# Kernel tuning notes

Measured on AMD Instinct MI355X. Metric: run time of the kernel, lower is better.

The kernel has to match this reference:

```python
import jax, jax.numpy as jnp
import numpy as np

N = 100000      # n_nodes
D = 64          # in_features == out_features (elementwise W mul requires equality)
DEG = 16        # avg degree for random edges
H = 2           # n_head
ALPHA = 0.2     # LeakyReLU negative slope


def setup_inputs() -> dict:
    key = jax.random.key(0)
    k1, k2, k3 = jax.random.split(key, 3)
    inputs = jax.random.normal(k1, (N, D), dtype=jnp.float32)
    # random edges + self-loops so every row has at least one edge (nonzero rowsum)
    rnd = jax.random.randint(k2, (2, N * DEG), 0, N)
    self_loops = jnp.tile(jnp.arange(N)[None, :], (2, 1))
    edge_index = jnp.concatenate([self_loops, rnd], axis=1)  # [2, 1.7M]
    # per-head params, matching torch init: W = ones, a ~ U(-stdv, stdv)
    W = jnp.ones((H, D), dtype=jnp.float32)
    stdv = 1.0 / np.sqrt(D * 2)
    a = jax.random.uniform(k3, (H, 2 * D), dtype=jnp.float32, minval=-stdv, maxval=stdv)
    return {"inputs": inputs, "edge_index": edge_index, "W": W, "a": a}


def reference(inputs, edge_index, W, a):
    n = inputs.shape[0]
    row, col = edge_index[0], edge_index[1]

    def head(Wh, ah):
        h = inputs * Wh  # [N, D]
        # a @ [h_src; h_dst] decomposes into per-node dots, then scalar edge gather
        score = (h @ ah[:D])[row] + (h @ ah[D:])[col]          # [E]
        e = jnp.exp(jnp.where(score > 0, score, ALPHA * score))  # exp(leaky_relu)
        rowsum = jax.ops.segment_sum(e, row, num_segments=n)     # [N]
        # sparse.mm(coo(edge, e), inputs): h_prime[i] = sum_j e_ij * inputs[j]
        h_prime = jax.ops.segment_sum(e[:, None] * inputs[col], row, num_segments=n)
        return h_prime / rowsum[:, None]

    outs = jax.vmap(head)(W, a)  # [H, N, D]
    return outs.mean(axis=0)
```

## Files before the change

kernel.cpp:

```cpp
#include <hip/hip_runtime.h>
#include <hip/hip_fp16.h>


#define D 64
#define ALPHA 0.2f
#define BSHIFT 8
#define BROWS 256
#define MAXBUK 512
#define TILE 2048
#define PK2 17
#define M17 ((1u << PK2) - 1u)
#define CAPE 6144

__device__ __forceinline__ unsigned bf16rne(float f) {
    unsigned u = __float_as_uint(f);
    u += 0x7fffu + ((u >> 16) & 1u);
    return u >> 16;
}
__device__ __forceinline__ float lrexp(float sc) {
    return __expf(sc > 0.f ? sc : ALPHA * sc);
}
__device__ __forceinline__ unsigned packe(float e0, float e1) {
    __half2 h = __floats2half2_rn(e0, e1);
    return *reinterpret_cast<unsigned*>(&h);
}
__device__ __forceinline__ float2 unpacke(unsigned u) {
    __half2 h = *reinterpret_cast<__half2*>(&u);
    return __half22float2(h);
}

__global__ __launch_bounds__(256) void k_front(
    const float* __restrict__ x, const float* __restrict__ W,
    const float* __restrict__ a, float4* __restrict__ s,
    unsigned* __restrict__ xh2, const int* __restrict__ row,
    unsigned short* __restrict__ tcnt, int N, int E, int nblkA)
{
    __shared__ int h[MAXBUK];
    if ((int)blockIdx.x < nblkA) {
        int wid  = (blockIdx.x * 256 + threadIdx.x) >> 6;
        int lane = threadIdx.x & 63;
        int node = wid * 4 + (lane >> 4);
        int f4   = lane & 15;
        if (node >= N) return;
        const float4* x4 = (const float4*)x;
        const float4* W4 = (const float4*)W;
        const float4* A4 = (const float4*)a;
        float4 v  = x4[(size_t)node * 16 + f4];
        unsigned u01 = (bf16rne(v.y) << 16) | bf16rne(v.x);
        unsigned u23 = (bf16rne(v.w) << 16) | bf16rne(v.z);
        *(uint2*)(xh2 + (size_t)node * 32 + 2 * f4) = make_uint2(u01, u23);
        float4 w0 = W4[f4], w1 = W4[16 + f4];
        float4 a0 = A4[f4], a1 = A4[16 + f4], a2 = A4[32 + f4], a3 = A4[48 + f4];
        float4 h0 = make_float4(v.x * w0.x, v.y * w0.y, v.z * w0.z, v.w * w0.w);
        float4 h1 = make_float4(v.x * w1.x, v.y * w1.y, v.z * w1.z, v.w * w1.w);
        float t0 = h0.x * a0.x + h0.y * a0.y + h0.z * a0.z + h0.w * a0.w;
        float t1 = h0.x * a1.x + h0.y * a1.y + h0.z * a1.z + h0.w * a1.w;
        float t2 = h1.x * a2.x + h1.y * a2.y + h1.z * a2.z + h1.w * a2.w;
        float t3 = h1.x * a3.x + h1.y * a3.y + h1.z * a3.z + h1.w * a3.w;
#pragma unroll
        for (int off = 1; off < 16; off <<= 1) {
            t0 += __shfl_xor(t0, off);
            t1 += __shfl_xor(t1, off);
            t2 += __shfl_xor(t2, off);
            t3 += __shfl_xor(t3, off);
        }
        if (f4 == 0) s[node] = make_float4(t0, t1, t2, t3);
    } else {
        int tile = blockIdx.x - nblkA;
        int t = threadIdx.x, base = tile * TILE;
        int cnt = E - base; if (cnt > TILE) cnt = TILE;
        h[t] = 0; h[t + 256] = 0;
        __syncthreads();
        for (int i = t; i < cnt; i += 256) atomicAdd(&h[row[base + i] >> BSHIFT], 1);
        __syncthreads();
        tcnt[(size_t)tile * MAXBUK + t]       = (unsigned short)h[t];
        tcnt[(size_t)tile * MAXBUK + t + 256] = (unsigned short)h[t + 256];
    }
}

__global__ __launch_bounds__(256) void k_col_scan(
    const unsigned short* __restrict__ tcnt, int* __restrict__ tbase,
    int* __restrict__ bcnt, int NT, int nbuk)
{
    int b = blockIdx.x, t = threadIdx.x;
    if (b >= nbuk) { if (t == 0) bcnt[b] = 0; return; }
    __shared__ int wsum[256];
    int t4 = t * 4;
    int v0 = (t4     < NT) ? tcnt[(size_t)(t4    ) * MAXBUK + b] : 0;
    int v1 = (t4 + 1 < NT) ? tcnt[(size_t)(t4 + 1) * MAXBUK + b] : 0;
    int v2 = (t4 + 2 < NT) ? tcnt[(size_t)(t4 + 2) * MAXBUK + b] : 0;
    int v3 = (t4 + 3 < NT) ? tcnt[(size_t)(t4 + 3) * MAXBUK + b] : 0;
    int sv = v0 + v1 + v2 + v3;
    wsum[t] = sv;
    __syncthreads();
    for (int off = 1; off < 256; off <<= 1) {
        int add = (t >= off) ? wsum[t - off] : 0;
        __syncthreads();
        wsum[t] += add;
        __syncthreads();
    }
    int run = wsum[t] - sv;
    if (t4     < NT) { tbase[(size_t)(t4    ) * MAXBUK + b] = run; run += v0; }
    if (t4 + 1 < NT) { tbase[(size_t)(t4 + 1) * MAXBUK + b] = run; run += v1; }
    if (t4 + 2 < NT) { tbase[(size_t)(t4 + 2) * MAXBUK + b] = run; run += v2; }
    if (t4 + 3 < NT) { tbase[(size_t)(t4 + 3) * MAXBUK + b] = run; run += v3; }
    if (t == 255) bcnt[b] = wsum[255];
}

__global__ __launch_bounds__(256) void k_binning(
    const int* __restrict__ row, const int* __restrict__ col,
    const unsigned short* __restrict__ tcnt, const int* __restrict__ bcnt,
    const int* __restrict__ tbase, unsigned* __restrict__ ebuf,
    int* __restrict__ bbase_g, int E)
{
    __shared__ int lrow[TILE];
    __shared__ int lcol[TILE];
    __shared__ int st[MAXBUK];
    __shared__ int gb[MAXBUK];
    __shared__ int cur[MAXBUK];
    __shared__ int w2[256];
    int t = threadIdx.x;
    int tile = blockIdx.x;
    int base = tile * TILE;
    int cnt = E - base; if (cnt > TILE) cnt = TILE;

    int h0 = tcnt[(size_t)tile * MAXBUK + 2 * t];
    int h1 = tcnt[(size_t)tile * MAXBUK + 2 * t + 1];
    int sv = h0 + h1;
    w2[t] = sv;
    __syncthreads();
    for (int off = 1; off < 256; off <<= 1) {
        int add = (t >= off) ? w2[t - off] : 0;
        __syncthreads();
        w2[t] += add;
        __syncthreads();
    }
    int run = w2[t] - sv;
    st[2 * t] = run;       st[2 * t + 1] = run + h0;
    cur[2 * t] = run;      cur[2 * t + 1] = run + h0;
    __syncthreads();

    int b0 = bcnt[2 * t], b1 = bcnt[2 * t + 1];
    int sb = b0 + b1;
    w2[t] = sb;
    __syncthreads();
    for (int off = 1; off < 256; off <<= 1) {
        int add = (t >= off) ? w2[t - off] : 0;
        __syncthreads();
        w2[t] += add;
        __syncthreads();
    }
    int runb = w2[t] - sb;
    gb[2 * t]     = runb      + tbase[(size_t)tile * MAXBUK + 2 * t];
    gb[2 * t + 1] = runb + b0 + tbase[(size_t)tile * MAXBUK + 2 * t + 1];
    if (tile == 0) {
        bbase_g[2 * t] = runb; bbase_g[2 * t + 1] = runb + b0;
        if (t == 255) bbase_g[512] = runb + b0 + b1;
    }
    __syncthreads();

    for (int i = t; i < cnt; i += 256) {
        int r = row[base + i], c = col[base + i];
        int p = atomicAdd(&cur[r >> BSHIFT], 1);
        lrow[p] = r; lcol[p] = c;
    }
    __syncthreads();

    for (int i = t; i < cnt; i += 256) {
        int rr = lrow[i];
        int bb = rr >> BSHIFT;
        ebuf[gb[bb] + (i - st[bb])] =
            ((unsigned)(rr & (BROWS - 1)) << PK2) | (unsigned)lcol[i];
    }
}

__global__ __launch_bounds__(1024) void k_rowsort(
    const unsigned* __restrict__ ebuf, const int* __restrict__ bbase,
    const float4* __restrict__ s, int* __restrict__ offsets,
    int* __restrict__ counts, unsigned* __restrict__ scol,
    __half* __restrict__ ecoef, int N)
{
    __shared__ unsigned lpk[CAPE];
    __shared__ unsigned lev[CAPE];
    __shared__ int   hist[BROWS];
    __shared__ int   offs[BROWS];
    __shared__ int   cursor[BROWS];
    __shared__ float rs0[BROWS], rs1[BROWS];
    __shared__ float rsx[BROWS], rsz[BROWS];
    __shared__ int   wsum[256];
    int b = blockIdx.x, t = threadIdx.x;
    int lo = b << BSHIFT;
    int s0 = bbase[b], s1 = bbase[b + 1];
    int seg = s1 - s0;

    if (t < BROWS) {
        int g = lo + t;
        float4 f = (g < N) ? s[g] : make_float4(0.f, 0.f, 0.f, 0.f);
        rsx[t] = f.x; rsz[t] = f.z;
        hist[t] = 0; rs0[t] = 0.f; rs1[t] = 0.f;
    }
    __syncthreads();

    for (int i = s0 + t; i < s1; i += 1024)
        atomicAdd(&hist[ebuf[i] >> PK2], 1);
    __syncthreads();

    int a = 0;
    if (t < BROWS) { a = hist[t]; wsum[t] = a; }
    __syncthreads();
    for (int off = 1; off < 256; off <<= 1) {
        int add = 0;
        if (t < BROWS && t >= off) add = wsum[t - off];
        __syncthreads();
        if (t < BROWS) wsum[t] += add;
        __syncthreads();
    }
    if (t < BROWS) { offs[t] = wsum[t] - a; cursor[t] = wsum[t] - a; }
    __syncthreads();

    if (seg <= CAPE) {
        for (int i = s0 + t; i < s1; i += 1024) {
            unsigned pk = ebuf[i];
            int r = pk >> PK2, c = (int)(pk & M17);
            float4 sc = s[c];
            float e0 = lrexp(rsx[r] + sc.y);
            float e1 = lrexp(rsz[r] + sc.w);
            atomicAdd(&rs0[r], e0);
            atomicAdd(&rs1[r], e1);
            int p = atomicAdd(&cursor[r], 1);
            lpk[p] = pk; lev[p] = packe(e0, e1);
        }
        __syncthreads();
        if (t < BROWS) {
            rs0[t] = 0.5f / rs0[t]; rs1[t] = 0.5f / rs1[t];
            int rg = lo + t;
            if (rg < N) { offsets[rg] = s0 + offs[t]; counts[rg] = hist[t]; }
        }
        __syncthreads();
        for (int i = t; i < seg; i += 1024) {
            unsigned pk = lpk[i];
            int r = pk >> PK2;
            float2 ef = unpacke(lev[i]);
            float coef = rs0[r] * ef.x + rs1[r] * ef.y;
            scol[s0 + i]  = (pk & M17) << 5;
            ecoef[s0 + i] = __float2half(coef);
        }
    } else {
        for (int i = s0 + t; i < s1; i += 1024) {
            unsigned pk = ebuf[i];
            int r = pk >> PK2, c = (int)(pk & M17);
            float4 sc = s[c];
            atomicAdd(&rs0[r], lrexp(rsx[r] + sc.y));
            atomicAdd(&rs1[r], lrexp(rsz[r] + sc.w));
        }
        __syncthreads();
        if (t < BROWS) {
            rs0[t] = 0.5f / rs0[t]; rs1[t] = 0.5f / rs1[t];
            int rg = lo + t;
            if (rg < N) { offsets[rg] = s0 + offs[t]; counts[rg] = hist[t]; }
        }
        __syncthreads();
        for (int i = s0 + t; i < s1; i += 1024) {
            unsigned pk = ebuf[i];
            int r = pk >> PK2, c = (int)(pk & M17);
            float4 sc = s[c];
            float coef = rs0[r] * lrexp(rsx[r] + sc.y)
                       + rs1[r] * lrexp(rsz[r] + sc.w);
            int p = atomicAdd(&cursor[r], 1);
            scol[s0 + p]  = (unsigned)c << 5;
            ecoef[s0 + p] = __float2half(coef);
        }
    }
}

__global__ __launch_bounds__(256) void k_gather(
    const unsigned* __restrict__ xh2, const int* __restrict__ offsets,
    const int* __restrict__ counts, const unsigned* __restrict__ scol,
    const __half* __restrict__ ecoef, float* __restrict__ out, int N)
{
    int w    = threadIdx.x >> 6;
    int lane = threadIdx.x & 63;
    int n    = blockIdx.x * 4 + w;
    if (n >= N) return;
    int start = offsets[n], cnt = counts[n];
    int q  = lane >> 4;
    int li = lane & 15;
    float a0 = 0.f, a1 = 0.f, a2 = 0.f, a3 = 0.f;
    for (int kk = q; kk < cnt; kk += 4) {
        unsigned cb = scol[start + kk];
        float cf = __half2float(ecoef[start + kk]);
        uint2 u = *(const uint2*)(xh2 + cb + 2 * li);
        a0 += cf * __uint_as_float(u.x << 16);
        a1 += cf * __uint_as_float(u.x & 0xffff0000u);
        a2 += cf * __uint_as_float(u.y << 16);
        a3 += cf * __uint_as_float(u.y & 0xffff0000u);
    }
    a0 += __shfl_xor(a0, 16); a0 += __shfl_xor(a0, 32);
    a1 += __shfl_xor(a1, 16); a1 += __shfl_xor(a1, 32);
    a2 += __shfl_xor(a2, 16); a2 += __shfl_xor(a2, 32);
    a3 += __shfl_xor(a3, 16); a3 += __shfl_xor(a3, 32);
    if (q == 0)
        ((float4*)(out + (size_t)n * D))[li] = make_float4(a0, a1, a2, a3);
}

extern "C" void kernel_launch(void* const* d_in, const int* in_sizes, int n_in,
                              void* d_out, int out_size, void* d_ws, size_t ws_size,
                              hipStream_t stream)
{
    const float* x  = (const float*)d_in[0];
    const int*   ei = (const int*)d_in[1];
    const float* W  = (const float*)d_in[2];
    const float* a  = (const float*)d_in[3];
    float*       out = (float*)d_out;
    int N = in_sizes[0] / D;
    int E = in_sizes[1] / 2;
    const int* row = ei;
    const int* col = ei + E;

    int NBUK = (N + BROWS - 1) >> BSHIFT;
    int NT   = (E + TILE - 1) / TILE;

    uintptr_t wp = (uintptr_t)d_ws;
    auto alloc = [&wp](size_t bytes) -> void* {
        wp = (wp + 255) & ~(uintptr_t)255;
        void* p = (void*)wp;
        wp += bytes;
        return p;
    };
    unsigned*       xh2     = (unsigned*)alloc((size_t)N * 32 * 4);
    float4*         s       = (float4*)alloc((size_t)N * sizeof(float4));
    int*            offsets = (int*)alloc((size_t)N * sizeof(int));
    int*            counts  = (int*)alloc((size_t)N * sizeof(int));
    unsigned*       scol    = (unsigned*)alloc((size_t)E * sizeof(unsigned));
    unsigned*       ebuf    = (unsigned*)alloc((size_t)E * sizeof(unsigned));
    __half*         ecoef   = (__half*)alloc((size_t)E * sizeof(__half));
    int*            tbase   = (int*)alloc((size_t)NT * MAXBUK * sizeof(int));
    int*            bcnt    = (int*)alloc(MAXBUK * sizeof(int));
    int*            bbase   = (int*)alloc((MAXBUK + 4) * sizeof(int));
    unsigned short* tcnt    = (unsigned short*)alloc((size_t)NT * MAXBUK * 2);

    int nblkA = (N + 15) / 16;
    k_front<<<nblkA + NT, 256, 0, stream>>>(x, W, a, s, xh2, row, tcnt, N, E, nblkA);
    k_col_scan<<<MAXBUK, 256, 0, stream>>>(tcnt, tbase, bcnt, NT, NBUK);
    k_binning<<<NT, 256, 0, stream>>>(row, col, tcnt, bcnt, tbase, ebuf, bbase, E);
    k_rowsort<<<NBUK, 1024, 0, stream>>>(ebuf, bbase, s, offsets, counts, scol, ecoef, N);
    k_gather<<<(N + 3) / 4, 256, 0, stream>>>(xh2, offsets, counts, scol, ecoef, out, N);
}
```

Before: 199.2 us.

## Drop global column scan; gather bucket segments per tile and stage neighbors in LDS

```diff
diff --git a/kernel.cpp b/kernel.cpp
--- a/kernel.cpp
+++ b/kernel.cpp
@@ -4,6 +4,7 @@
 
 #define D 64
 #define ALPHA 0.2f
+#define CAP 96
 #define BSHIFT 8
 #define BROWS 256
 #define MAXBUK 512
@@ -11,6 +12,7 @@
 #define PK2 17
 #define M17 ((1u << PK2) - 1u)
 #define CAPE 6144
+#define SSTR 8192
 
 __device__ __forceinline__ unsigned bf16rne(float f) {
     unsigned u = __float_as_uint(f);
@@ -51,12 +53,10 @@
         *(uint2*)(xh2 + (size_t)node * 32 + 2 * f4) = make_uint2(u01, u23);
         float4 w0 = W4[f4], w1 = W4[16 + f4];
         float4 a0 = A4[f4], a1 = A4[16 + f4], a2 = A4[32 + f4], a3 = A4[48 + f4];
-        float4 h0 = make_float4(v.x * w0.x, v.y * w0.y, v.z * w0.z, v.w * w0.w);
-        float4 h1 = make_float4(v.x * w1.x, v.y * w1.y, v.z * w1.z, v.w * w1.w);
-        float t0 = h0.x * a0.x + h0.y * a0.y + h0.z * a0.z + h0.w * a0.w;
-        float t1 = h0.x * a1.x + h0.y * a1.y + h0.z * a1.z + h0.w * a1.w;
-        float t2 = h1.x * a2.x + h1.y * a2.y + h1.z * a2.z + h1.w * a2.w;
-        float t3 = h1.x * a3.x + h1.y * a3.y + h1.z * a3.z + h1.w * a3.w;
+        float t0 = v.x*w0.x*a0.x + v.y*w0.y*a0.y + v.z*w0.z*a0.z + v.w*w0.w*a0.w;
+        float t1 = v.x*w0.x*a1.x + v.y*w0.y*a1.y + v.z*w0.z*a1.z + v.w*w0.w*a1.w;
+        float t2 = v.x*w1.x*a2.x + v.y*w1.y*a2.y + v.z*w1.z*a2.z + v.w*w1.w*a2.w;
+        float t3 = v.x*w1.x*a3.x + v.y*w1.y*a3.y + v.z*w1.z*a3.z + v.w*w1.w*a3.w;
 #pragma unroll
         for (int off = 1; off < 16; off <<= 1) {
             t0 += __shfl_xor(t0, off);
@@ -78,120 +78,58 @@
     }
 }
 
-__global__ __launch_bounds__(256) void k_col_scan(
-    const unsigned short* __restrict__ tcnt, int* __restrict__ tbase,
-    int* __restrict__ bcnt, int NT, int nbuk)
-{
-    int b = blockIdx.x, t = threadIdx.x;
-    if (b >= nbuk) { if (t == 0) bcnt[b] = 0; return; }
-    __shared__ int wsum[256];
-    int t4 = t * 4;
-    int v0 = (t4     < NT) ? tcnt[(size_t)(t4    ) * MAXBUK + b] : 0;
-    int v1 = (t4 + 1 < NT) ? tcnt[(size_t)(t4 + 1) * MAXBUK + b] : 0;
-    int v2 = (t4 + 2 < NT) ? tcnt[(size_t)(t4 + 2) * MAXBUK + b] : 0;
-    int v3 = (t4 + 3 < NT) ? tcnt[(size_t)(t4 + 3) * MAXBUK + b] : 0;
-    int sv = v0 + v1 + v2 + v3;
-    wsum[t] = sv;
-    __syncthreads();
-    for (int off = 1; off < 256; off <<= 1) {
-        int add = (t >= off) ? wsum[t - off] : 0;
-        __syncthreads();
-        wsum[t] += add;
-        __syncthreads();
-    }
-    int run = wsum[t] - sv;
-    if (t4     < NT) { tbase[(size_t)(t4    ) * MAXBUK + b] = run; run += v0; }
-    if (t4 + 1 < NT) { tbase[(size_t)(t4 + 1) * MAXBUK + b] = run; run += v1; }
-    if (t4 + 2 < NT) { tbase[(size_t)(t4 + 2) * MAXBUK + b] = run; run += v2; }
-    if (t4 + 3 < NT) { tbase[(size_t)(t4 + 3) * MAXBUK + b] = run; run += v3; }
-    if (t == 255) bcnt[b] = wsum[255];
-}
-
 __global__ __launch_bounds__(256) void k_binning(
     const int* __restrict__ row, const int* __restrict__ col,
-    const unsigned short* __restrict__ tcnt, const int* __restrict__ bcnt,
-    const int* __restrict__ tbase, unsigned* __restrict__ ebuf,
-    int* __restrict__ bbase_g, int E)
-{
-    __shared__ int lrow[TILE];
-    __shared__ int lcol[TILE];
-    __shared__ int st[MAXBUK];
-    __shared__ int gb[MAXBUK];
+    const unsigned short* __restrict__ tcnt, unsigned* __restrict__ ebuf,
+    unsigned* __restrict__ tmeta, int E)
+{
+    __shared__ unsigned lpk[TILE];
     __shared__ int cur[MAXBUK];
-    __shared__ int w2[256];
-    int t = threadIdx.x;
-    int tile = blockIdx.x;
-    int base = tile * TILE;
+    __shared__ int wsum[256];
+    int t = threadIdx.x, tile = blockIdx.x, base = tile * TILE;
     int cnt = E - base; if (cnt > TILE) cnt = TILE;
 
     int h0 = tcnt[(size_t)tile * MAXBUK + 2 * t];
     int h1 = tcnt[(size_t)tile * MAXBUK + 2 * t + 1];
     int sv = h0 + h1;
-    w2[t] = sv;
+    wsum[t] = sv;
     __syncthreads();
     for (int off = 1; off < 256; off <<= 1) {
-        int add = (t >= off) ? w2[t - off] : 0;
-        __syncthreads();
-        w2[t] += add;
-        __syncthreads();
-    }
-    int run = w2[t] - sv;
-    st[2 * t] = run;       st[2 * t + 1] = run + h0;
-    cur[2 * t] = run;      cur[2 * t + 1] = run + h0;
-    __syncthreads();
-
-    int b0 = bcnt[2 * t], b1 = bcnt[2 * t + 1];
-    int sb = b0 + b1;
-    w2[t] = sb;
-    __syncthreads();
-    for (int off = 1; off < 256; off <<= 1) {
-        int add = (t >= off) ? w2[t - off] : 0;
-        __syncthreads();
-        w2[t] += add;
-        __syncthreads();
-    }
-    int runb = w2[t] - sb;
-    gb[2 * t]     = runb      + tbase[(size_t)tile * MAXBUK + 2 * t];
-    gb[2 * t + 1] = runb + b0 + tbase[(size_t)tile * MAXBUK + 2 * t + 1];
-    if (tile == 0) {
-        bbase_g[2 * t] = runb; bbase_g[2 * t + 1] = runb + b0;
-        if (t == 255) bbase_g[512] = runb + b0 + b1;
-    }
+        int add = (t >= off) ? wsum[t - off] : 0;
+        __syncthreads();
+        wsum[t] += add;
+        __syncthreads();
+    }
+    int run = wsum[t] - sv;
+    cur[2 * t] = run;  cur[2 * t + 1] = run + h0;
+    tmeta[(size_t)tile * MAXBUK + 2 * t]     = ((unsigned)run << 16) | (unsigned)h0;
+    tmeta[(size_t)tile * MAXBUK + 2 * t + 1] = ((unsigned)(run + h0) << 16) | (unsigned)h1;
     __syncthreads();
 
     for (int i = t; i < cnt; i += 256) {
         int r = row[base + i], c = col[base + i];
         int p = atomicAdd(&cur[r >> BSHIFT], 1);
-        lrow[p] = r; lcol[p] = c;
-    }
-    __syncthreads();
-
-    for (int i = t; i < cnt; i += 256) {
-        int rr = lrow[i];
-        int bb = rr >> BSHIFT;
-        ebuf[gb[bb] + (i - st[bb])] =
-            ((unsigned)(rr & (BROWS - 1)) << PK2) | (unsigned)lcol[i];
-    }
+        lpk[p] = ((unsigned)(r & (BROWS - 1)) << PK2) | (unsigned)c;
+    }
+    __syncthreads();
+    for (int i = t; i < cnt; i += 256) ebuf[base + i] = lpk[i];
 }
 
 __global__ __launch_bounds__(1024) void k_rowsort(
-    const unsigned* __restrict__ ebuf, const int* __restrict__ bbase,
+    const unsigned* __restrict__ ebuf, const unsigned* __restrict__ tmeta,
     const float4* __restrict__ s, int* __restrict__ offsets,
     int* __restrict__ counts, unsigned* __restrict__ scol,
-    __half* __restrict__ ecoef, int N)
-{
-    __shared__ unsigned lpk[CAPE];
-    __shared__ unsigned lev[CAPE];
-    __shared__ int   hist[BROWS];
-    __shared__ int   offs[BROWS];
-    __shared__ int   cursor[BROWS];
-    __shared__ float rs0[BROWS], rs1[BROWS];
-    __shared__ float rsx[BROWS], rsz[BROWS];
+    __half* __restrict__ ecoef, int NT, int N)
+{
+    __shared__ unsigned lpkA[CAPE];
+    __shared__ unsigned lpkB[CAPE];
+    __shared__ unsigned levB[CAPE];
+    __shared__ int   hist[BROWS], offs[BROWS], cursor[BROWS];
+    __shared__ float rs0[BROWS], rs1[BROWS], rsx[BROWS], rsz[BROWS];
     __shared__ int   wsum[256];
+    __shared__ int   top;
     int b = blockIdx.x, t = threadIdx.x;
     int lo = b << BSHIFT;
-    int s0 = bbase[b], s1 = bbase[b + 1];
-    int seg = s1 - s0;
 
     if (t < BROWS) {
         int g = lo + t;
@@ -199,28 +137,41 @@
         rsx[t] = f.x; rsz[t] = f.z;
         hist[t] = 0; rs0[t] = 0.f; rs1[t] = 0.f;
     }
-    __syncthreads();
-
-    for (int i = s0 + t; i < s1; i += 1024)
-        atomicAdd(&hist[ebuf[i] >> PK2], 1);
-    __syncthreads();
-
-    int a = 0;
-    if (t < BROWS) { a = hist[t]; wsum[t] = a; }
-    __syncthreads();
-    for (int off = 1; off < 256; off <<= 1) {
-        int add = 0;
-        if (t < BROWS && t >= off) add = wsum[t - off];
-        __syncthreads();
-        if (t < BROWS) wsum[t] += add;
-        __syncthreads();
-    }
-    if (t < BROWS) { offs[t] = wsum[t] - a; cursor[t] = wsum[t] - a; }
-    __syncthreads();
+    if (t == 0) top = 0;
+    __syncthreads();
+
+    int myh = 0, mybase = 0, mydst = 0;
+    if (t < NT) {
+        unsigned m = tmeta[(size_t)t * MAXBUK + b];
+        myh = (int)(m & 0xffffu);
+        mybase = t * TILE + (int)(m >> 16);
+        if (myh) mydst = atomicAdd(&top, myh);
+    }
+    __syncthreads();
+    int seg = top;
+    size_t ob = (size_t)b * SSTR;
 
     if (seg <= CAPE) {
-        for (int i = s0 + t; i < s1; i += 1024) {
-            unsigned pk = ebuf[i];
+        for (int j = 0; j < myh; j++) {
+            unsigned pk = ebuf[mybase + j];
+            lpkA[mydst + j] = pk;
+            atomicAdd(&hist[pk >> PK2], 1);
+        }
+        __syncthreads();
+        int a = 0;
+        if (t < 256) { a = hist[t]; wsum[t] = a; }
+        __syncthreads();
+        for (int off = 1; off < 256; off <<= 1) {
+            int add = 0;
+            if (t < 256 && t >= off) add = wsum[t - off];
+            __syncthreads();
+            if (t < 256) wsum[t] += add;
+            __syncthreads();
+        }
+        if (t < 256) { offs[t] = wsum[t] - a; cursor[t] = wsum[t] - a; }
+        __syncthreads();
+        for (int i = t; i < seg; i += 1024) {
+            unsigned pk = lpkA[i];
             int r = pk >> PK2, c = (int)(pk & M17);
             float4 sc = s[c];
             float e0 = lrexp(rsx[r] + sc.y);
@@ -228,47 +179,61 @@
             atomicAdd(&rs0[r], e0);
             atomicAdd(&rs1[r], e1);
             int p = atomicAdd(&cursor[r], 1);
-            lpk[p] = pk; lev[p] = packe(e0, e1);
+            lpkB[p] = pk; levB[p] = packe(e0, e1);
         }
         __syncthreads();
         if (t < BROWS) {
             rs0[t] = 0.5f / rs0[t]; rs1[t] = 0.5f / rs1[t];
             int rg = lo + t;
-            if (rg < N) { offsets[rg] = s0 + offs[t]; counts[rg] = hist[t]; }
+            if (rg < N) { offsets[rg] = (int)ob + offs[t]; counts[rg] = hist[t]; }
         }
         __syncthreads();
         for (int i = t; i < seg; i += 1024) {
-            unsigned pk = lpk[i];
+            unsigned pk = lpkB[i];
             int r = pk >> PK2;
-            float2 ef = unpacke(lev[i]);
-            float coef = rs0[r] * ef.x + rs1[r] * ef.y;
-            scol[s0 + i]  = (pk & M17) << 5;
-            ecoef[s0 + i] = __float2half(coef);
+            float2 ef = unpacke(levB[i]);
+            scol[ob + i]  = (pk & M17) << 5;
+            ecoef[ob + i] = __float2half(rs0[r] * ef.x + rs1[r] * ef.y);
         }
     } else {
-        for (int i = s0 + t; i < s1; i += 1024) {
-            unsigned pk = ebuf[i];
+        for (int j = 0; j < myh; j++) {
+            unsigned pk = ebuf[mybase + j];
             int r = pk >> PK2, c = (int)(pk & M17);
             float4 sc = s[c];
             atomicAdd(&rs0[r], lrexp(rsx[r] + sc.y));
             atomicAdd(&rs1[r], lrexp(rsz[r] + sc.w));
-        }
+            atomicAdd(&hist[r], 1);
+        }
+        __syncthreads();
+        int a = 0;
+        if (t < 256) { a = hist[t]; wsum[t] = a; }
+        __syncthreads();
+        for (int off = 1; off < 256; off <<= 1) {
+            int add = 0;
+            if (t < 256 && t >= off) add = wsum[t - off];
+            __syncthreads();
+            if (t < 256) wsum[t] += add;
+            __syncthreads();
+        }
+        if (t < 256) { offs[t] = wsum[t] - a; cursor[t] = wsum[t] - a; }
         __syncthreads();
         if (t < BROWS) {
             rs0[t] = 0.5f / rs0[t]; rs1[t] = 0.5f / rs1[t];
             int rg = lo + t;
-            if (rg < N) { offsets[rg] = s0 + offs[t]; counts[rg] = hist[t]; }
-        }
-        __syncthreads();
-        for (int i = s0 + t; i < s1; i += 1024) {
-            unsigned pk = ebuf[i];
+            if (rg < N) { offsets[rg] = (int)ob + offs[t]; counts[rg] = hist[t]; }
+        }
+        __syncthreads();
+        for (int j = 0; j < myh; j++) {
+            unsigned pk = ebuf[mybase + j];
             int r = pk >> PK2, c = (int)(pk & M17);
             float4 sc = s[c];
             float coef = rs0[r] * lrexp(rsx[r] + sc.y)
                        + rs1[r] * lrexp(rsz[r] + sc.w);
             int p = atomicAdd(&cursor[r], 1);
-            scol[s0 + p]  = (unsigned)c << 5;
-            ecoef[s0 + p] = __float2half(coef);
+            if ((unsigned)p < SSTR) {
+                scol[ob + p]  = (unsigned)(pk & M17) << 5;
+                ecoef[ob + p] = __float2half(coef);
+            }
         }
     }
 }
@@ -278,17 +243,40 @@
     const int* __restrict__ counts, const unsigned* __restrict__ scol,
     const __half* __restrict__ ecoef, float* __restrict__ out, int N)
 {
+    __shared__ unsigned lc[4][CAP];
+    __shared__ float    lf[4][CAP];
     int w    = threadIdx.x >> 6;
     int lane = threadIdx.x & 63;
     int n    = blockIdx.x * 4 + w;
     if (n >= N) return;
     int start = offsets[n], cnt = counts[n];
+    int m = cnt < CAP ? cnt : CAP;
+    for (int k = lane; k < m; k += 64) {
+        lc[w][k] = scol[start + k];
+        lf[w][k] = __half2float(ecoef[start + k]);
+    }
+    int mp = (m + 7) & ~7;
+    { int k = m + lane; if (k < mp) { lc[w][k] = 0; lf[w][k] = 0.f; } }
+
     int q  = lane >> 4;
     int li = lane & 15;
     float a0 = 0.f, a1 = 0.f, a2 = 0.f, a3 = 0.f;
-    for (int kk = q; kk < cnt; kk += 4) {
+    for (int k = 0; k < mp; k += 8) {
+#pragma unroll
+        for (int j = 0; j < 2; j++) {
+            int kk = k + 4 * j + q;
+            unsigned cb = lc[w][kk];
+            float    cf = lf[w][kk];
+            uint2 u = *(const uint2*)(xh2 + cb + 2 * li);
+            a0 += cf * __uint_as_float(u.x << 16);
+            a1 += cf * __uint_as_float(u.x & 0xffff0000u);
+            a2 += cf * __uint_as_float(u.y << 16);
+            a3 += cf * __uint_as_float(u.y & 0xffff0000u);
+        }
+    }
+    for (int kk = CAP + q; kk < cnt; kk += 4) {
         unsigned cb = scol[start + kk];
-        float cf = __half2float(ecoef[start + kk]);
+        float    cf = __half2float(ecoef[start + kk]);
         uint2 u = *(const uint2*)(xh2 + cb + 2 * li);
         a0 += cf * __uint_as_float(u.x << 16);
         a1 += cf * __uint_as_float(u.x & 0xffff0000u);
@@ -331,18 +319,15 @@
     float4*         s       = (float4*)alloc((size_t)N * sizeof(float4));
     int*            offsets = (int*)alloc((size_t)N * sizeof(int));
     int*            counts  = (int*)alloc((size_t)N * sizeof(int));
-    unsigned*       scol    = (unsigned*)alloc((size_t)E * sizeof(unsigned));
     unsigned*       ebuf    = (unsigned*)alloc((size_t)E * sizeof(unsigned));
-    __half*         ecoef   = (__half*)alloc((size_t)E * sizeof(__half));
-    int*            tbase   = (int*)alloc((size_t)NT * MAXBUK * sizeof(int));
-    int*            bcnt    = (int*)alloc(MAXBUK * sizeof(int));
-    int*            bbase   = (int*)alloc((MAXBUK + 4) * sizeof(int));
+    unsigned*       scol    = (unsigned*)alloc((size_t)NBUK * SSTR * sizeof(unsigned));
+    __half*         ecoef   = (__half*)alloc((size_t)NBUK * SSTR * sizeof(__half));
+    unsigned*       tmeta   = (unsigned*)alloc((size_t)NT * MAXBUK * sizeof(unsigned));
     unsigned short* tcnt    = (unsigned short*)alloc((size_t)NT * MAXBUK * 2);
 
     int nblkA = (N + 15) / 16;
     k_front<<<nblkA + NT, 256, 0, stream>>>(x, W, a, s, xh2, row, tcnt, N, E, nblkA);
-    k_col_scan<<<MAXBUK, 256, 0, stream>>>(tcnt, tbase, bcnt, NT, NBUK);
-    k_binning<<<NT, 256, 0, stream>>>(row, col, tcnt, bcnt, tbase, ebuf, bbase, E);
-    k_rowsort<<<NBUK, 1024, 0, stream>>>(ebuf, bbase, s, offsets, counts, scol, ecoef, N);
+    k_binning<<<NT, 256, 0, stream>>>(row, col, tcnt, ebuf, tmeta, E);
+    k_rowsort<<<NBUK, 1024, 0, stream>>>(ebuf, tmeta, s, offsets, counts, scol, ecoef, NT, N);
     k_gather<<<(N + 3) / 4, 256, 0, stream>>>(xh2, offsets, counts, scol, ecoef, out, N);
 }
```

Result: no change. 200.6 us (+0.7%).
